# Performance work log

Hardware: AMD Instinct MI355X
Metric: run time of the kernel (lower is better)

Reference implementation:

```python
import jax, jax.numpy as jnp
import numpy as np

B, N, D = 8, 1024, 1024
H, DQK, DV = 8, 128, 128
L, TB = 2, 128
LN_EPS = 1e-6
LOG2 = 0.69314718056


def _layer_norm(x, g, b):
    mu = jnp.mean(x, axis=-1, keepdims=True)
    var = jnp.mean(jnp.square(x - mu), axis=-1, keepdims=True)
    return (x - mu) * jax.lax.rsqrt(var + LN_EPS) * g + b


def setup_inputs() -> dict:
    key = jax.random.key(0)
    ks = jax.random.split(key, 8)
    x = 0.02 * jax.random.normal(ks[0], (B, N, D), dtype=jnp.float32)
    timestamps = jnp.sort(jax.random.randint(ks[1], (B, N), 0, 10_000_000), axis=1).astype(jnp.int64)
    lengths = jax.random.randint(ks[2], (B,), N // 4, N + 1)
    mask = (jnp.arange(N)[None, :] < lengths[:, None]).astype(jnp.float32)  # ragged prefix mask
    return {
        "x": x,
        "timestamps": timestamps,
        "mask": mask,
        "ln1_g": jnp.ones((L, D), jnp.float32),
        "ln1_b": jnp.zeros((L, D), jnp.float32),
        "w_uvqk": 0.02 * jax.random.normal(ks[3], (L, D, 2 * H * DV + 2 * H * DQK), jnp.float32),
        "b_uvqk": jnp.zeros((L, 2 * H * DV + 2 * H * DQK), jnp.float32),
        "ln2_g": jnp.ones((L, H * DV), jnp.float32),
        "ln2_b": jnp.zeros((L, H * DV), jnp.float32),
        "w_o": 0.02 * jax.random.normal(ks[4], (L, H * DV, D), jnp.float32),
        "b_o": jnp.zeros((L, D), jnp.float32),
        "pos_w": 0.02 * jax.random.normal(ks[5], (2 * N - 1,), jnp.float32),
        "ts_w": 0.02 * jax.random.normal(ks[6], (TB + 1,), jnp.float32),
    }


def _forward(x, timestamps, mask, ln1_g, ln1_b, w_uvqk, b_uvqk, ln2_g, ln2_b, w_o, b_o, pos_w, ts_w):
    # relative position bias: pos_w[(n - m) + N - 1]
    i = jnp.arange(N)
    rel_pos = pos_w[jnp.clip(i[:, None] - i[None, :] + N - 1, 0, 2 * N - 2)]  # [N, N]
    # bucketized relative time bias (log2 bucketization, detached indices)
    ext = jnp.concatenate([timestamps, timestamps[:, -1:]], axis=1)  # [B, N+1]
    delta = ext[:, 1:, None] - ext[:, None, :-1]  # [B, N, N]
    bucket = jnp.clip(
        (jnp.log(jnp.clip(jnp.abs(delta).astype(jnp.float32), 1.0, None)) / LOG2).astype(jnp.int32),
        0, TB)
    rab = rel_pos[None, :, :] + ts_w[bucket]  # [B, N, N]
    # causal * key-validity mask (invalid_attn_mask = 1 - triu; jagged padding is zero)
    amask = jnp.tril(jnp.ones((N, N), x.dtype))[None] * mask[:, None, :]  # [B, N, N]
    x = x * mask[..., None]
    for l in range(L):
        h = _layer_norm(x, ln1_g[l], ln1_b[l])
        uvqk = jax.nn.silu(h @ w_uvqk[l] + b_uvqk[l])  # [B, N, 4096]
        u = uvqk[..., : H * DV]
        v = uvqk[..., H * DV: 2 * H * DV].reshape(B, N, H, DV)
        q = uvqk[..., 2 * H * DV: 2 * H * DV + H * DQK].reshape(B, N, H, DQK)
        k = uvqk[..., 2 * H * DV + H * DQK:].reshape(B, N, H, DQK)
        attn = jax.nn.silu(jnp.einsum('bnhd,bmhd->bhnm', q, k) + rab[:, None]) / N
        attn = attn * amask[:, None]
        o = jnp.einsum('bhnm,bmhd->bnhd', attn, v).reshape(B, N, H * DV)
        x = x + (_layer_norm(o, ln2_g[l], ln2_b[l]) * u) @ w_o[l] + b_o[l]
    # F.normalize(p=2)
    ue = x / jnp.clip(jnp.linalg.norm(x, axis=-1, keepdims=True), 1e-12)
    lengths = mask.sum(axis=1).astype(jnp.int32)  # [B]
    last = ue[jnp.arange(B), lengths - 1]  # gather last valid token, [B, D]
    avg = (ue * mask[..., None]).sum(axis=1) / lengths[:, None].astype(ue.dtype)
    pooled = 0.5 * (last + avg)
    pooled = pooled / jnp.clip(jnp.linalg.norm(pooled, axis=-1, keepdims=True), 1e-12)
    return pooled


def reference(x, timestamps, mask, ln1_g, ln1_b, w_uvqk, b_uvqk, ln2_g, ln2_b, w_o, b_o, pos_w, ts_w):
    return _forward(x, timestamps, mask, ln1_g, ln1_b, w_uvqk, b_uvqk, ln2_g, ln2_b, w_o, b_o, pos_w, ts_w)
```

## Files before the change

### kernel.cpp

```cpp
#include <hip/hip_runtime.h>
#include <hip/hip_bf16.h>
#include <cstdint>
#include <cstddef>


#define BB   8
#define NNN  1024
#define DDD  1024
#define HHH  8
#define DVV  128
#define CCC  4096
#define TBK  128

typedef __bf16 bf8_t  __attribute__((ext_vector_type(8)));
typedef float  f4_t   __attribute__((ext_vector_type(4)));

__device__ __forceinline__ float bf2f(ushort u) {
  union { uint i; float f; } v; v.i = ((uint)u) << 16; return v.f;
}
__device__ __forceinline__ ushort f2bf(float f) {
  __hip_bfloat16 h = __float2bfloat16(f);
  return *(ushort*)&h;
}

__device__ __forceinline__ float block_reduce_sum(float v, float* sm) {
#pragma unroll
  for (int o = 32; o > 0; o >>= 1) v += __shfl_down(v, o, 64);
  int lane = threadIdx.x & 63;
  int wid  = threadIdx.x >> 6;
  __syncthreads();
  if (lane == 0) sm[wid] = v;
  __syncthreads();
  int nw = blockDim.x >> 6;
  float r = (threadIdx.x < nw) ? sm[threadIdx.x] : 0.f;
#pragma unroll
  for (int o = 8; o > 0; o >>= 1) r += __shfl_down(r, o, 64);
  if (threadIdx.x == 0) sm[0] = r;
  __syncthreads();
  return sm[0];
}

__global__ __launch_bounds__(1024) void len_k(const float* __restrict__ mask,
                                              int* __restrict__ lenp) {
  __shared__ float sm[16];
  int b = blockIdx.x;
  float m = mask[(size_t)b * NNN + threadIdx.x];
  float s = block_reduce_sum(m, sm);
  if (threadIdx.x == 0) lenp[b] = (int)(s + 0.5f);
}

__global__ __launch_bounds__(256) void wconv_k(const float* __restrict__ W,
                                               ushort* __restrict__ Wt,
                                               int K, int Nn) {
  __shared__ float t[32][33];
  int k0 = blockIdx.x * 32, n0 = blockIdx.y * 32;
  int tx = threadIdx.x & 31, ty = threadIdx.x >> 5;
  for (int r = ty; r < 32; r += 8)
    t[r][tx] = W[(size_t)(k0 + r) * Nn + n0 + tx];
  __syncthreads();
  for (int r = ty; r < 32; r += 8)
    Wt[(size_t)(n0 + r) * K + k0 + tx] = f2bf(t[tx][r]);
}

__global__ __launch_bounds__(256) void rab_k(const int* __restrict__ ts,
                                             const float* __restrict__ pos_w,
                                             const float* __restrict__ ts_w,
                                             const int* __restrict__ lenp,
                                             ushort* __restrict__ rabb) {
  int jt = blockIdx.x, it = blockIdx.y, b = blockIdx.z;
  if (jt > it) return;
  int len = lenp[b];
  if (it * 128 >= len || jt * 128 >= len) return;
  int j = jt * 128 + (threadIdx.x & 127);
  int half = threadIdx.x >> 7;
  int tsj = ts[(size_t)b * NNN + j];
  for (int rr = 0; rr < 64; ++rr) {
    int i = it * 128 + rr * 2 + half;
    int ii = i + 1; if (ii > NNN - 1) ii = NNN - 1;
    int tsi = ts[(size_t)b * NNN + ii];
    float af = fabsf((float)(tsi - tsj));
    af = fmaxf(af, 1.f);
    int bkt = (int)__log2f(af);
    bkt = min(max(bkt, 0), TBK);
    float rab = pos_w[i - j + NNN - 1] + ts_w[bkt];
    rabb[((size_t)b * NNN + i) * NNN + j] = f2bf(rab);
  }
}

template <int FIRST>
__global__ __launch_bounds__(256) void ln_k(const float* __restrict__ X,
                                            const float* __restrict__ g,
                                            const float* __restrict__ bsh,
                                            const float* __restrict__ umat,
                                            int ustride,
                                            const int* __restrict__ lenp,
                                            float* __restrict__ xb,
                                            ushort* __restrict__ Y) {
  __shared__ float sm[16];
  size_t row = blockIdx.x;
  if (((int)row & 1023) >= lenp[row >> 10]) return;
  const float* xr = X + row * DDD;
  int d = threadIdx.x * 4;
  float4 xv = *(const float4*)(xr + d);
  if (FIRST) *(float4*)(xb + row * DDD + d) = xv;
  float s = xv.x + xv.y + xv.z + xv.w;
  s = block_reduce_sum(s, sm);
  float mu = s * (1.f / 1024.f);
  float d0 = xv.x - mu, d1 = xv.y - mu, d2 = xv.z - mu, d3 = xv.w - mu;
  float ss = d0 * d0 + d1 * d1 + d2 * d2 + d3 * d3;
  ss = block_reduce_sum(ss, sm);
  float rs = rsqrtf(ss * (1.f / 1024.f) + 1e-6f);
  float y0 = d0 * rs * g[d + 0] + bsh[d + 0];
  float y1 = d1 * rs * g[d + 1] + bsh[d + 1];
  float y2 = d2 * rs * g[d + 2] + bsh[d + 2];
  float y3 = d3 * rs * g[d + 3] + bsh[d + 3];
  if (umat != nullptr) {
    const float* ur = umat + row * (size_t)ustride + d;
    y0 *= ur[0]; y1 *= ur[1]; y2 *= ur[2]; y3 *= ur[3];
  }
  ushort tmp[4] = { f2bf(y0), f2bf(y1), f2bf(y2), f2bf(y3) };
  *(uint2*)(Y + row * DDD + d) = *(uint2*)tmp;
}

template <int MODE>
__global__ __launch_bounds__(256) void gemm_bf_k(const ushort* __restrict__ A,
                                                 const ushort* __restrict__ Bt,
                                                 const float* __restrict__ bias,
                                                 float* __restrict__ C,
                                                 ushort* __restrict__ Qk,
                                                 ushort* __restrict__ Vt,
                                                 const int* __restrict__ lenp,
                                                 int K, int Nn) {
  __shared__ alignas(16) ushort As[2 * 128 * 32];
  __shared__ alignas(16) ushort Bs[2 * 128 * 32];
  int m0 = blockIdx.y * 128, n0 = blockIdx.x * 128;
  if ((m0 & 1023) >= lenp[m0 >> 10]) return;
  int tid = threadIdx.x;
  int wave = tid >> 6, lane = tid & 63;
  int quad = lane >> 4, l16 = lane & 15;
  int wm = wave >> 1, wn = wave & 1;

  f4_t acc[4][4] = {};

  int r_l = tid >> 2;
  int p   = tid & 3;

  for (int k0 = 0; k0 < K; k0 += 64) {
    __syncthreads();
#pragma unroll
    for (int s = 0; s < 2; ++s) {
#pragma unroll
      for (int g = 0; g < 2; ++g) {
        int row = g * 64 + r_l;
        int q = (p - (row >> 1)) & 3;
        __builtin_amdgcn_global_load_lds(
            (const __attribute__((address_space(1))) void*)(A + (size_t)(m0 + row) * K + k0 + s * 32 + q * 8),
            (__attribute__((address_space(3))) void*)(As + s * 4096 + (g * 64 + wave * 16) * 32),
            16, 0, 0);
        __builtin_amdgcn_global_load_lds(
            (const __attribute__((address_space(1))) void*)(Bt + (size_t)(n0 + row) * K + k0 + s * 32 + q * 8),
            (__attribute__((address_space(3))) void*)(Bs + s * 4096 + (g * 64 + wave * 16) * 32),
            16, 0, 0);
      }
    }
    __syncthreads();

#pragma unroll
    for (int s = 0; s < 2; ++s) {
      bf8_t af[4], bfr[4];
#pragma unroll
      for (int t = 0; t < 4; ++t) {
        int row = wm * 64 + t * 16 + l16;
        af[t] = *(const bf8_t*)&As[s * 4096 + row * 32 + ((quad + (row >> 1)) & 3) * 8];
        int col = wn * 64 + t * 16 + l16;
        bfr[t] = *(const bf8_t*)&Bs[s * 4096 + col * 32 + ((quad + (col >> 1)) & 3) * 8];
      }
#pragma unroll
      for (int i = 0; i < 4; ++i)
#pragma unroll
        for (int j = 0; j < 4; ++j)
          acc[i][j] = __builtin_amdgcn_mfma_f32_16x16x32_bf16(af[i], bfr[j],
                                                              acc[i][j], 0, 0, 0);
    }
  }

  int region = n0 >> 10;
#pragma unroll
  for (int j = 0; j < 4; ++j) {
    int col = n0 + wn * 64 + j * 16 + l16;
    float bz = bias[col];
#pragma unroll
    for (int i = 0; i < 4; ++i) {
      int rbase = m0 + wm * 64 + i * 16 + quad * 4;
      if (MODE == 1) {
#pragma unroll
        for (int r = 0; r < 4; ++r)
          C[(size_t)(rbase + r) * Nn + col] += acc[i][j][r] + bz;
      } else if (region == 0) {
#pragma unroll
        for (int r = 0; r < 4; ++r) {
          float z = acc[i][j][r] + bz;
          C[(size_t)(rbase + r) * 1024 + col] = z / (1.f + __expf(-z));
        }
      } else if (region == 1) {
        int hd = col - 1024;
        int b = m0 >> 10, nl = rbase & 1023;
        ushort4 pk;
        float z;
        z = acc[i][j][0] + bz; pk.x = f2bf(z / (1.f + __expf(-z)));
        z = acc[i][j][1] + bz; pk.y = f2bf(z / (1.f + __expf(-z)));
        z = acc[i][j][2] + bz; pk.z = f2bf(z / (1.f + __expf(-z)));
        z = acc[i][j][3] + bz; pk.w = f2bf(z / (1.f + __expf(-z)));
        *(ushort4*)&Vt[((size_t)(b * 8 + (hd >> 7)) * 128 + (hd & 127)) * NNN + nl] = pk;
      } else {
#pragma unroll
        for (int r = 0; r < 4; ++r) {
          float z = acc[i][j][r] + bz;
          Qk[(size_t)(rbase + r) * 2048 + (col - 2048)] = f2bf(z / (1.f + __expf(-z)));
        }
      }
    }
  }
}

__global__ __launch_bounds__(256, 4) void attn_mfma_k(
    const ushort* __restrict__ qk, const ushort* __restrict__ vt,
    const ushort* __restrict__ rabb, const float* __restrict__ mask,
    const int* __restrict__ lenp, float* __restrict__ o) {
  __shared__ alignas(16) ushort Ks[64 * 128];
  __shared__ alignas(16) ushort Vs[128 * 64];
  __shared__ alignas(16) ushort Ps[64 * 64];
  int h = blockIdx.y, b = blockIdx.z;
  int qt = ((int)blockIdx.x + (int)blockIdx.y + 2 * (int)blockIdx.z) & 15;
  int n0 = qt * 64;
  if (n0 >= lenp[b]) return;
  int tid = threadIdx.x, w = tid >> 6, lane = tid & 63;
  int quad = lane >> 4, l16 = lane & 15;

  const ushort* qg0 = qk + ((size_t)(b * NNN + n0)) * 2048 + h * 128;
#pragma unroll
  for (int t = 0; t < 4; ++t) {
    int lrow = w * 16 + t * 4 + (lane >> 4);
    int q = ((lane & 15) - lrow) & 15;
    __builtin_amdgcn_global_load_lds(
        (const __attribute__((address_space(1))) void*)(qg0 + (size_t)lrow * 2048 + q * 8),
        (__attribute__((address_space(3))) void*)(Ks + (w * 16 + t * 4) * 128),
        16, 0, 0);
  }
  __syncthreads();
  bf8_t qf[4];
  {
    int lr = w * 16 + l16;
#pragma unroll
    for (int kk = 0; kk < 4; ++kk)
      qf[kk] = *(const bf8_t*)&Ks[lr * 128 + (((kk * 4 + quad) + lr) & 15) * 8];
  }

  f4_t oacc[8] = {};
  const ushort* kg0 = qk + (size_t)b * NNN * 2048 + 1024 + h * 128;
  const ushort* vg0 = vt + (size_t)(b * 8 + h) * 128 * NNN;
  const ushort* rb0 = rabb + ((size_t)(b * NNN + n0 + w * 16 + quad * 4)) * NNN;
  const float* mk0 = mask + (size_t)b * NNN;
  int mtmax = qt + 1;

  for (int mt = 0; mt < mtmax; ++mt) {
    int m0 = mt * 64;
    __syncthreads();
#pragma unroll
    for (int t = 0; t < 4; ++t) {
      int lrow = w * 16 + t * 4 + (lane >> 4);
      int q = ((lane & 15) - lrow) & 15;
      __builtin_amdgcn_global_load_lds(
          (const __attribute__((address_space(1))) void*)(kg0 + (size_t)(m0 + lrow) * 2048 + q * 8),
          (__attribute__((address_space(3))) void*)(Ks + (w * 16 + t * 4) * 128),
          16, 0, 0);
    }
#pragma unroll
    for (int t = 0; t < 4; ++t) {
      int dv = w * 32 + t * 8 + (lane >> 3);
      int q = ((lane & 7) - dv) & 7;
      __builtin_amdgcn_global_load_lds(
          (const __attribute__((address_space(1))) void*)(vg0 + (size_t)dv * NNN + m0 + q * 8),
          (__attribute__((address_space(3))) void*)(Vs + (w * 32 + t * 8) * 64),
          16, 0, 0);
    }
    ushort rv[4][4];
#pragma unroll
    for (int tj = 0; tj < 4; ++tj)
#pragma unroll
      for (int r = 0; r < 4; ++r)
        rv[tj][r] = rb0[(size_t)r * NNN + m0 + tj * 16 + l16];
    __syncthreads();

    f4_t sacc[4] = {};
#pragma unroll
    for (int kk = 0; kk < 4; ++kk) {
      bf8_t kf[4];
#pragma unroll
      for (int tj = 0; tj < 4; ++tj) {
        int lr = tj * 16 + l16;
        kf[tj] = *(const bf8_t*)&Ks[lr * 128 + (((kk * 4 + quad) + lr) & 15) * 8];
      }
#pragma unroll
      for (int tj = 0; tj < 4; ++tj)
        sacc[tj] = __builtin_amdgcn_mfma_f32_16x16x32_bf16(qf[kk], kf[tj],
                                                           sacc[tj], 0, 0, 0);
    }

#pragma unroll
    for (int tj = 0; tj < 4; ++tj) {
      int m = tj * 16 + l16;
      int gj = m0 + m;
      float msc = mk0[gj] * (1.f / 1024.f);
#pragma unroll
      for (int r = 0; r < 4; ++r) {
        int q = w * 16 + quad * 4 + r;
        int gi = n0 + q;
        float z = sacc[tj][r] + bf2f(rv[tj][r]);
        float pp = z / (1.f + __expf(-z)) * msc;
        if (gj > gi) pp = 0.f;
        Ps[q * 64 + (((m >> 3) + q) & 7) * 8 + (m & 7)] = f2bf(pp);
      }
    }

#pragma unroll
    for (int kk = 0; kk < 2; ++kk) {
      bf8_t pf, vf[8];
      {
        int q = w * 16 + l16;
        pf = *(const bf8_t*)&Ps[q * 64 + (((kk * 4 + quad) + q) & 7) * 8];
      }
#pragma unroll
      for (int tj = 0; tj < 8; ++tj) {
        int dv = tj * 16 + l16;
        vf[tj] = *(const bf8_t*)&Vs[dv * 64 + (((kk * 4 + quad) + dv) & 7) * 8];
      }
#pragma unroll
      for (int tj = 0; tj < 8; ++tj)
        oacc[tj] = __builtin_amdgcn_mfma_f32_16x16x32_bf16(pf, vf[tj],
                                                           oacc[tj], 0, 0, 0);
    }
  }

#pragma unroll
  for (int tj = 0; tj < 8; ++tj) {
    int col = h * 128 + tj * 16 + l16;
#pragma unroll
    for (int r = 0; r < 4; ++r) {
      int gi = n0 + w * 16 + quad * 4 + r;
      o[((size_t)(b * NNN + gi)) * DDD + col] = oacc[tj][r];
    }
  }
}

__global__ __launch_bounds__(256) void row_stats_k(const float* __restrict__ xb,
                                                   const int* __restrict__ lenp,
                                                   float* __restrict__ invn) {
  __shared__ float sm[16];
  size_t row = blockIdx.x;
  if (((int)row & 1023) >= lenp[row >> 10]) return;
  int d = threadIdx.x * 4;
  float4 xv = *(const float4*)(xb + row * DDD + d);
  float ss = xv.x * xv.x + xv.y * xv.y + xv.z * xv.z + xv.w * xv.w;
  ss = block_reduce_sum(ss, sm);
  if (threadIdx.x == 0) invn[row] = 1.f / fmaxf(sqrtf(ss), 1e-12f);
}

__global__ __launch_bounds__(1024) void pool_partial_k(const float* __restrict__ xb,
                                                       const float* __restrict__ invn,
                                                       const int* __restrict__ lenp,
                                                       float* __restrict__ partial) {
  int b = blockIdx.x, c = blockIdx.y, d = threadIdx.x;
  int len = lenp[b];
  float s = 0.f;
  int nbeg = c * 64;
  int nend = min(nbeg + 64, len);
  for (int n = nbeg; n < nend; ++n) {
    size_t r = (size_t)b * NNN + n;
    s += xb[r * DDD + d] * invn[r];
  }
  partial[((size_t)b * 16 + c) * DDD + d] = s;
}

__global__ __launch_bounds__(1024) void pool_final_k(const float* __restrict__ xb,
                                                     const float* __restrict__ invn,
                                                     const float* __restrict__ partial,
                                                     const int* __restrict__ lenp,
                                                     float* __restrict__ out) {
  __shared__ float sm[16];
  int b = blockIdx.x, d = threadIdx.x;
  int len = lenp[b];
  float s = 0.f;
#pragma unroll
  for (int c = 0; c < 16; ++c) s += partial[((size_t)b * 16 + c) * DDD + d];
  float avg = s / (float)len;
  size_t lr = (size_t)b * NNN + (len - 1);
  float last = xb[lr * DDD + d] * invn[lr];
  float pooled = 0.5f * (last + avg);
  float ssq = block_reduce_sum(pooled * pooled, sm);
  out[(size_t)b * DDD + d] = pooled / fmaxf(sqrtf(ssq), 1e-12f);
}

extern "C" void kernel_launch(void* const* d_in, const int* in_sizes, int n_in,
                              void* d_out, int out_size, void* d_ws, size_t ws_size,
                              hipStream_t stream) {
  const float* x      = (const float*)d_in[0];
  const int*   ts     = (const int*)d_in[1];
  const float* mask   = (const float*)d_in[2];
  const float* ln1_g  = (const float*)d_in[3];
  const float* ln1_b  = (const float*)d_in[4];
  const float* w_uvqk = (const float*)d_in[5];
  const float* b_uvqk = (const float*)d_in[6];
  const float* ln2_g  = (const float*)d_in[7];
  const float* ln2_b  = (const float*)d_in[8];
  const float* w_o    = (const float*)d_in[9];
  const float* b_o    = (const float*)d_in[10];
  const float* pos_w  = (const float*)d_in[11];
  const float* ts_w   = (const float*)d_in[12];
  float* out = (float*)d_out;

  float* ws = (float*)d_ws;
  const size_t SZ = (size_t)BB * NNN * DDD;
  float* xb   = ws;
  float* buf1 = ws + SZ;
  float* ubuf = ws + 2 * SZ;
  ushort* hbf = (ushort*)(ws + 3 * SZ);
  ushort* wuT = hbf + SZ;
  ushort* woT = wuT + 2 * (size_t)DDD * CCC;
  ushort* qkb = woT + 2 * (size_t)DDD * DDD;
  ushort* vtb = qkb + (size_t)BB * NNN * 2048;
  ushort* rabb = vtb + (size_t)BB * HHH * DVV * NNN;
  float* invn = (float*)(rabb + (size_t)BB * NNN * NNN);
  float* partial = invn + (size_t)BB * NNN;
  int* lenp = (int*)(partial + (size_t)BB * 16 * DDD);

  len_k<<<BB, 1024, 0, stream>>>(mask, lenp);

  for (int l = 0; l < 2; ++l) {
    wconv_k<<<dim3(DDD / 32, CCC / 32), 256, 0, stream>>>(
        w_uvqk + (size_t)l * DDD * CCC, wuT + (size_t)l * CCC * DDD, DDD, CCC);
    wconv_k<<<dim3(DDD / 32, DDD / 32), 256, 0, stream>>>(
        w_o + (size_t)l * DDD * DDD, woT + (size_t)l * DDD * DDD, DDD, DDD);
  }

  rab_k<<<dim3(8, 8, BB), 256, 0, stream>>>(ts, pos_w, ts_w, lenp, rabb);

  for (int l = 0; l < 2; ++l) {
    if (l == 0)
      ln_k<1><<<BB * NNN, 256, 0, stream>>>(x, ln1_g, ln1_b, nullptr, 0,
                                            lenp, xb, hbf);
    else
      ln_k<0><<<BB * NNN, 256, 0, stream>>>(xb, ln1_g + l * DDD,
                                            ln1_b + l * DDD, nullptr, 0,
                                            lenp, nullptr, hbf);
    gemm_bf_k<2><<<dim3(CCC / 128, BB * NNN / 128), 256, 0, stream>>>(
        hbf, wuT + (size_t)l * CCC * DDD, b_uvqk + (size_t)l * CCC,
        ubuf, qkb, vtb, lenp, DDD, CCC);
    attn_mfma_k<<<dim3(NNN / 64, HHH, BB), 256, 0, stream>>>(
        qkb, vtb, rabb, mask, lenp, buf1);
    ln_k<0><<<BB * NNN, 256, 0, stream>>>(buf1, ln2_g + l * DDD,
                                          ln2_b + l * DDD, ubuf, DDD,
                                          lenp, nullptr, hbf);
    gemm_bf_k<1><<<dim3(DDD / 128, BB * NNN / 128), 256, 0, stream>>>(
        hbf, woT + (size_t)l * DDD * DDD, b_o + (size_t)l * DDD,
        xb, nullptr, nullptr, lenp, DDD, DDD);
  }

  row_stats_k<<<BB * NNN, 256, 0, stream>>>(xb, lenp, invn);
  pool_partial_k<<<dim3(BB, 16), 1024, 0, stream>>>(xb, invn, lenp, partial);
  pool_final_k<<<BB, 1024, 0, stream>>>(xb, invn, partial, lenp, out);
}
```

Before: 670.0 us.

## Stage GEMM epilogue through LDS for coalesced stores and store U as bf16

```diff
diff --git a/kernel.cpp b/kernel.cpp
--- a/kernel.cpp
+++ b/kernel.cpp
@@ -14,6 +14,7 @@
 
 typedef __bf16 bf8_t  __attribute__((ext_vector_type(8)));
 typedef float  f4_t   __attribute__((ext_vector_type(4)));
+typedef ushort us8_t  __attribute__((ext_vector_type(8)));
 
 __device__ __forceinline__ float bf2f(ushort u) {
   union { uint i; float f; } v; v.i = ((uint)u) << 16; return v.f;
@@ -21,6 +22,9 @@
 __device__ __forceinline__ ushort f2bf(float f) {
   __hip_bfloat16 h = __float2bfloat16(f);
   return *(ushort*)&h;
+}
+__device__ __forceinline__ float silu(float z) {
+  return z / (1.f + __expf(-z));
 }
 
 __device__ __forceinline__ float block_reduce_sum(float v, float* sm) {
@@ -49,17 +53,28 @@
   if (threadIdx.x == 0) lenp[b] = (int)(s + 0.5f);
 }
 
-__global__ __launch_bounds__(256) void wconv_k(const float* __restrict__ W,
-                                               ushort* __restrict__ Wt,
-                                               int K, int Nn) {
+__global__ __launch_bounds__(256) void wconv_all_k(const float* __restrict__ w_uvqk,
+                                                   const float* __restrict__ w_o,
+                                                   ushort* __restrict__ wuT,
+                                                   ushort* __restrict__ woT) {
   __shared__ float t[32][33];
-  int k0 = blockIdx.x * 32, n0 = blockIdx.y * 32;
+  int l = blockIdx.z;
+  int k0 = blockIdx.x * 32;
+  int by = blockIdx.y;
+  const float* W; ushort* Wt; int Nn, n0;
+  if (by < 128) {
+    W = w_uvqk + (size_t)l * DDD * CCC; Wt = wuT + (size_t)l * CCC * DDD;
+    Nn = CCC; n0 = by * 32;
+  } else {
+    W = w_o + (size_t)l * DDD * DDD; Wt = woT + (size_t)l * DDD * DDD;
+    Nn = DDD; n0 = (by - 128) * 32;
+  }
   int tx = threadIdx.x & 31, ty = threadIdx.x >> 5;
   for (int r = ty; r < 32; r += 8)
     t[r][tx] = W[(size_t)(k0 + r) * Nn + n0 + tx];
   __syncthreads();
   for (int r = ty; r < 32; r += 8)
-    Wt[(size_t)(n0 + r) * K + k0 + tx] = f2bf(t[tx][r]);
+    Wt[(size_t)(n0 + r) * 1024 + k0 + tx] = f2bf(t[tx][r]);
 }
 
 __global__ __launch_bounds__(256) void rab_k(const int* __restrict__ ts,
@@ -91,8 +106,7 @@
 __global__ __launch_bounds__(256) void ln_k(const float* __restrict__ X,
                                             const float* __restrict__ g,
                                             const float* __restrict__ bsh,
-                                            const float* __restrict__ umat,
-                                            int ustride,
+                                            const ushort* __restrict__ umat,
                                             const int* __restrict__ lenp,
                                             float* __restrict__ xb,
                                             ushort* __restrict__ Y) {
@@ -115,8 +129,8 @@
   float y2 = d2 * rs * g[d + 2] + bsh[d + 2];
   float y3 = d3 * rs * g[d + 3] + bsh[d + 3];
   if (umat != nullptr) {
-    const float* ur = umat + row * (size_t)ustride + d;
-    y0 *= ur[0]; y1 *= ur[1]; y2 *= ur[2]; y3 *= ur[3];
+    ushort4 uv = *(const ushort4*)(umat + row * 1024 + d);
+    y0 *= bf2f(uv.x); y1 *= bf2f(uv.y); y2 *= bf2f(uv.z); y3 *= bf2f(uv.w);
   }
   ushort tmp[4] = { f2bf(y0), f2bf(y1), f2bf(y2), f2bf(y3) };
   *(uint2*)(Y + row * DDD + d) = *(uint2*)tmp;
@@ -127,12 +141,16 @@
                                                  const ushort* __restrict__ Bt,
                                                  const float* __restrict__ bias,
                                                  float* __restrict__ C,
+                                                 ushort* __restrict__ U,
                                                  ushort* __restrict__ Qk,
                                                  ushort* __restrict__ Vt,
                                                  const int* __restrict__ lenp,
                                                  int K, int Nn) {
-  __shared__ alignas(16) ushort As[2 * 128 * 32];
-  __shared__ alignas(16) ushort Bs[2 * 128 * 32];
+  __shared__ alignas(16) char smem[64 * 132 * 4];
+  ushort* As = (ushort*)smem;
+  ushort* Bs = As + 128 * 32;
+  float*  eps = (float*)smem;
+
   int m0 = blockIdx.y * 128, n0 = blockIdx.x * 128;
   if ((m0 & 1023) >= lenp[m0 >> 10]) return;
   int tid = threadIdx.x;
@@ -145,79 +163,100 @@
   int r_l = tid >> 2;
   int p   = tid & 3;
 
-  for (int k0 = 0; k0 < K; k0 += 64) {
+  for (int k0 = 0; k0 < K; k0 += 32) {
     __syncthreads();
 #pragma unroll
-    for (int s = 0; s < 2; ++s) {
-#pragma unroll
-      for (int g = 0; g < 2; ++g) {
-        int row = g * 64 + r_l;
-        int q = (p - (row >> 1)) & 3;
-        __builtin_amdgcn_global_load_lds(
-            (const __attribute__((address_space(1))) void*)(A + (size_t)(m0 + row) * K + k0 + s * 32 + q * 8),
-            (__attribute__((address_space(3))) void*)(As + s * 4096 + (g * 64 + wave * 16) * 32),
-            16, 0, 0);
-        __builtin_amdgcn_global_load_lds(
-            (const __attribute__((address_space(1))) void*)(Bt + (size_t)(n0 + row) * K + k0 + s * 32 + q * 8),
-            (__attribute__((address_space(3))) void*)(Bs + s * 4096 + (g * 64 + wave * 16) * 32),
-            16, 0, 0);
+    for (int g = 0; g < 2; ++g) {
+      int row = g * 64 + r_l;
+      int q = (p - (row >> 1)) & 3;
+      __builtin_amdgcn_global_load_lds(
+          (const __attribute__((address_space(1))) void*)(A + (size_t)(m0 + row) * K + k0 + q * 8),
+          (__attribute__((address_space(3))) void*)(As + (g * 64 + wave * 16) * 32),
+          16, 0, 0);
+      __builtin_amdgcn_global_load_lds(
+          (const __attribute__((address_space(1))) void*)(Bt + (size_t)(n0 + row) * K + k0 + q * 8),
+          (__attribute__((address_space(3))) void*)(Bs + (g * 64 + wave * 16) * 32),
+          16, 0, 0);
+    }
+    __syncthreads();
+
+    bf8_t af[4], bfr[4];
+#pragma unroll
+    for (int t = 0; t < 4; ++t) {
+      int row = wm * 64 + t * 16 + l16;
+      af[t] = *(const bf8_t*)&As[row * 32 + ((quad + (row >> 1)) & 3) * 8];
+      int col = wn * 64 + t * 16 + l16;
+      bfr[t] = *(const bf8_t*)&Bs[col * 32 + ((quad + (col >> 1)) & 3) * 8];
+    }
+#pragma unroll
+    for (int i = 0; i < 4; ++i)
+#pragma unroll
+      for (int j = 0; j < 4; ++j)
+        acc[i][j] = __builtin_amdgcn_mfma_f32_16x16x32_bf16(af[i], bfr[j],
+                                                            acc[i][j], 0, 0, 0);
+  }
+
+  int region = (MODE == 2) ? (n0 >> 10) : -1;
+#pragma unroll
+  for (int ph = 0; ph < 2; ++ph) {
+    __syncthreads();
+    if (wm == ph) {
+#pragma unroll
+      for (int i = 0; i < 4; ++i)
+#pragma unroll
+        for (int j = 0; j < 4; ++j)
+#pragma unroll
+          for (int r = 0; r < 4; ++r)
+            eps[(i * 16 + quad * 4 + r) * 132 + wn * 64 + j * 16 + l16] =
+                acc[i][j][r];
+    }
+    __syncthreads();
+
+    int mbase = m0 + ph * 64;
+    if (MODE == 1 || region == 0 || region >= 2) {
+      int row = tid >> 2;
+      int c0 = (tid & 3) * 4;
+      int gr = mbase + row;
+      const float* er = eps + row * 132;
+#pragma unroll
+      for (int s = 0; s < 8; ++s) {
+        int col = c0 + s * 16;
+        float4 b4 = *(const float4*)(bias + n0 + col);
+        float z0 = er[col + 0] + b4.x;
+        float z1 = er[col + 1] + b4.y;
+        float z2 = er[col + 2] + b4.z;
+        float z3 = er[col + 3] + b4.w;
+        if (MODE == 1) {
+          float* cp = C + (size_t)gr * Nn + n0 + col;
+          float4 c4 = *(const float4*)cp;
+          c4.x += z0; c4.y += z1; c4.z += z2; c4.w += z3;
+          *(float4*)cp = c4;
+        } else {
+          ushort4 pk;
+          pk.x = f2bf(silu(z0)); pk.y = f2bf(silu(z1));
+          pk.z = f2bf(silu(z2)); pk.w = f2bf(silu(z3));
+          if (region == 0)
+            *(ushort4*)(U + (size_t)gr * 1024 + n0 + col) = pk;
+          else
+            *(ushort4*)(Qk + (size_t)gr * 2048 + (n0 + col - 2048)) = pk;
+        }
       }
-    }
-    __syncthreads();
-
-#pragma unroll
-    for (int s = 0; s < 2; ++s) {
-      bf8_t af[4], bfr[4];
-#pragma unroll
-      for (int t = 0; t < 4; ++t) {
-        int row = wm * 64 + t * 16 + l16;
-        af[t] = *(const bf8_t*)&As[s * 4096 + row * 32 + ((quad + (row >> 1)) & 3) * 8];
-        int col = wn * 64 + t * 16 + l16;
-        bfr[t] = *(const bf8_t*)&Bs[s * 4096 + col * 32 + ((quad + (col >> 1)) & 3) * 8];
-      }
-#pragma unroll
-      for (int i = 0; i < 4; ++i)
-#pragma unroll
-        for (int j = 0; j < 4; ++j)
-          acc[i][j] = __builtin_amdgcn_mfma_f32_16x16x32_bf16(af[i], bfr[j],
-                                                              acc[i][j], 0, 0, 0);
-    }
-  }
-
-  int region = n0 >> 10;
-#pragma unroll
-  for (int j = 0; j < 4; ++j) {
-    int col = n0 + wn * 64 + j * 16 + l16;
-    float bz = bias[col];
-#pragma unroll
-    for (int i = 0; i < 4; ++i) {
-      int rbase = m0 + wm * 64 + i * 16 + quad * 4;
-      if (MODE == 1) {
-#pragma unroll
-        for (int r = 0; r < 4; ++r)
-          C[(size_t)(rbase + r) * Nn + col] += acc[i][j][r] + bz;
-      } else if (region == 0) {
-#pragma unroll
-        for (int r = 0; r < 4; ++r) {
-          float z = acc[i][j][r] + bz;
-          C[(size_t)(rbase + r) * 1024 + col] = z / (1.f + __expf(-z));
+    } else {
+      int col = tid & 127;
+      int half = tid >> 7;
+      float bz = bias[n0 + col];
+      int hb = (n0 >> 7) & 7;
+      ushort* vrow = Vt + (((size_t)((m0 >> 10) * 8 + hb)) * 128 + col) * NNN +
+                     (mbase & 1023) + half * 32;
+#pragma unroll
+      for (int g = 0; g < 4; ++g) {
+        us8_t pk;
+#pragma unroll
+        for (int e = 0; e < 8; ++e) {
+          int r = half * 32 + g * 8 + e;
+          pk[e] = f2bf(silu(eps[r * 132 + col] + bz));
         }
-      } else if (region == 1) {
-        int hd = col - 1024;
-        int b = m0 >> 10, nl = rbase & 1023;
-        ushort4 pk;
-        float z;
-        z = acc[i][j][0] + bz; pk.x = f2bf(z / (1.f + __expf(-z)));
-        z = acc[i][j][1] + bz; pk.y = f2bf(z / (1.f + __expf(-z)));
-        z = acc[i][j][2] + bz; pk.z = f2bf(z / (1.f + __expf(-z)));
-        z = acc[i][j][3] + bz; pk.w = f2bf(z / (1.f + __expf(-z)));
-        *(ushort4*)&Vt[((size_t)(b * 8 + (hd >> 7)) * 128 + (hd & 127)) * NNN + nl] = pk;
-      } else {
-#pragma unroll
-        for (int r = 0; r < 4; ++r) {
-          float z = acc[i][j][r] + bz;
-          Qk[(size_t)(rbase + r) * 2048 + (col - 2048)] = f2bf(z / (1.f + __expf(-z)));
-        }
+        *(us8_t*)(vrow + g * 8) = pk;
       }
     }
   }
@@ -317,7 +356,7 @@
         int q = w * 16 + quad * 4 + r;
         int gi = n0 + q;
         float z = sacc[tj][r] + bf2f(rv[tj][r]);
-        float pp = z / (1.f + __expf(-z)) * msc;
+        float pp = silu(z) * msc;
         if (gj > gi) pp = 0.f;
         Ps[q * 64 + (((m >> 3) + q) & 7) * 8 + (m & 7)] = f2bf(pp);
       }
@@ -423,7 +462,7 @@
   const size_t SZ = (size_t)BB * NNN * DDD;
   float* xb   = ws;
   float* buf1 = ws + SZ;
-  float* ubuf = ws + 2 * SZ;
+  ushort* ubuf = (ushort*)(ws + 2 * SZ);
   ushort* hbf = (ushort*)(ws + 3 * SZ);
   ushort* wuT = hbf + SZ;
   ushort* woT = wuT + 2 * (size_t)DDD * CCC;
@@ -435,35 +474,28 @@
   int* lenp = (int*)(partial + (size_t)BB * 16 * DDD);
 
   len_k<<<BB, 1024, 0, stream>>>(mask, lenp);
-
-  for (int l = 0; l < 2; ++l) {
-    wconv_k<<<dim3(DDD / 32, CCC / 32), 256, 0, stream>>>(
-        w_uvqk + (size_t)l * DDD * CCC, wuT + (size_t)l * CCC * DDD, DDD, CCC);
-    wconv_k<<<dim3(DDD / 32, DDD / 32), 256, 0, stream>>>(
-        w_o + (size_t)l * DDD * DDD, woT + (size_t)l * DDD * DDD, DDD, DDD);
-  }
-
+  wconv_all_k<<<dim3(32, 160, 2), 256, 0, stream>>>(w_uvqk, w_o, wuT, woT);
   rab_k<<<dim3(8, 8, BB), 256, 0, stream>>>(ts, pos_w, ts_w, lenp, rabb);
 
   for (int l = 0; l < 2; ++l) {
     if (l == 0)
-      ln_k<1><<<BB * NNN, 256, 0, stream>>>(x, ln1_g, ln1_b, nullptr, 0,
+      ln_k<1><<<BB * NNN, 256, 0, stream>>>(x, ln1_g, ln1_b, nullptr,
                                             lenp, xb, hbf);
     else
       ln_k<0><<<BB * NNN, 256, 0, stream>>>(xb, ln1_g + l * DDD,
-                                            ln1_b + l * DDD, nullptr, 0,
+                                            ln1_b + l * DDD, nullptr,
                                             lenp, nullptr, hbf);
     gemm_bf_k<2><<<dim3(CCC / 128, BB * NNN / 128), 256, 0, stream>>>(
         hbf, wuT + (size_t)l * CCC * DDD, b_uvqk + (size_t)l * CCC,
-        ubuf, qkb, vtb, lenp, DDD, CCC);
+        nullptr, ubuf, qkb, vtb, lenp, DDD, CCC);
     attn_mfma_k<<<dim3(NNN / 64, HHH, BB), 256, 0, stream>>>(
         qkb, vtb, rabb, mask, lenp, buf1);
     ln_k<0><<<BB * NNN, 256, 0, stream>>>(buf1, ln2_g + l * DDD,
-                                          ln2_b + l * DDD, ubuf, DDD,
+                                          ln2_b + l * DDD, ubuf,
                                           lenp, nullptr, hbf);
     gemm_bf_k<1><<<dim3(DDD / 128, BB * NNN / 128), 256, 0, stream>>>(
         hbf, woT + (size_t)l * DDD * DDD, b_o + (size_t)l * DDD,
-        xb, nullptr, nullptr, lenp, DDD, DDD);
+        xb, nullptr, nullptr, nullptr, lenp, DDD, DDD);
   }
 
   row_stats_k<<<BB * NNN, 256, 0, stream>>>(xb, lenp, invn);
```

After: 631.5 us. 5.7% less time.
